# Optimization experiments

Measured on AMD Instinct MI355X. Metric: run time of the kernel, lower is better.

## Reference

```python
import jax, jax.numpy as jnp
import numpy as np

TEMPERATURE = 8.0  # sqrt(d_k) with d_k = 64


def setup_inputs() -> dict:
    key = jax.random.key(0)
    kq, kk, kv = jax.random.split(key, 3)
    B, L, D = 64, 1024, 64
    q = jax.random.normal(kq, (B, L, D), dtype=jnp.float32)
    k = jax.random.normal(kk, (B, L, D), dtype=jnp.float32)
    v = jax.random.normal(kv, (B, L, D), dtype=jnp.float32)
    return {"q": q, "k": k, "v": v}


def reference(q, k, v):
    # attn = q @ k^T / temperature  -> [B, Lq, Lk]
    attn = jnp.einsum("bqd,bkd->bqk", q, k) / TEMPERATURE
    attn = jax.nn.softmax(attn, axis=2)
    # output = attn @ v -> [B, Lq, Dv]  (dropout is identity in eval mode)
    out = jnp.einsum("bqk,bkd->bqd", attn, v)
    return out
```

## Files before the change

### kernel.cpp

```cpp
#include <hip/hip_runtime.h>
#include <hip/hip_bf16.h>

#define L_SEQ 1024
#define NT 32

typedef __attribute__((ext_vector_type(8))) __bf16 bf16x8;
typedef __attribute__((ext_vector_type(4))) __bf16 bf16x4;
typedef __attribute__((ext_vector_type(4))) float f32x4;

__device__ __forceinline__ float fast_exp2(float x) {
#if __has_builtin(__builtin_amdgcn_exp2f)
    return __builtin_amdgcn_exp2f(x);
#else
    return exp2f(x);
#endif
}

#define MFMA16(a, b, c) __builtin_amdgcn_mfma_f32_16x16x32_bf16((a), (b), (c), 0, 0, 0)

__global__ __launch_bounds__(512) void sdpa_fused(
    const float* __restrict__ Q, const float* __restrict__ K,
    const float* __restrict__ V, float* __restrict__ O)
{
    __shared__ __align__(16) char lds[2 * 8192];

    const int tid  = threadIdx.x;
    const int lane = tid & 63;
    const int wave = tid >> 6;
    const int li   = lane & 15;
    const int h    = lane >> 4;

    const int wg = blockIdx.x;
    const int lb = (wg & 7) * 64 + (wg >> 3);
    const int b  = lb >> 3;
    const int qt = lb & 7;
    const int q0 = qt * 128 + wave * 16 + li;

    const float* Qb = Q + (size_t)b * L_SEQ * 64;
    const char*  Kb = (const char*)(K + (size_t)b * L_SEQ * 64);
    const float* Vf = V + (size_t)b * L_SEQ * 64;

    int kd0;
    {
        const int qi = tid;
        const int r  = qi >> 4;
        const int d4 = (qi & 15) << 2;
        const int c32 = d4 >> 5, rem = d4 & 31, hf = rem >> 4, hh = (rem & 15) >> 2;
        kd0 = r * 128 + 2 * (((c32 * 32 + hh * 8) ^ ((r & 7) * 8)) + hf * 4);
    }
    const int vd  = tid & 63;
    const int vwd = 4096 + vd * 64 + 8 * (wave ^ ((vd >> 1) & 7));

    const float QSC = 0.18033688011112042f;
    bf16x8 qf0, qf1;
    {
        const float* ra = &Qb[(size_t)q0 * 64];
        f32x4 a00 = *(const f32x4*)&ra[0  + h * 4];
        f32x4 a01 = *(const f32x4*)&ra[16 + h * 4];
        f32x4 a10 = *(const f32x4*)&ra[32 + h * 4];
        f32x4 a11 = *(const f32x4*)&ra[48 + h * 4];
        #pragma unroll
        for (int j = 0; j < 4; ++j) {
            qf0[j]     = (__bf16)(a00[j] * QSC);
            qf0[4 + j] = (__bf16)(a01[j] * QSC);
            qf1[j]     = (__bf16)(a10[j] * QSC);
            qf1[4 + j] = (__bf16)(a11[j] * QSC);
        }
    }

    bf16x8 ones;
    #pragma unroll
    for (int j = 0; j < 8; ++j) ones[j] = (__bf16)1.0f;

    const float NBIAS = -46.0f;
    f32x4 o0 = {0.f,0.f,0.f,0.f}, o1 = {0.f,0.f,0.f,0.f};
    f32x4 o2 = {0.f,0.f,0.f,0.f}, o3 = {0.f,0.f,0.f,0.f};
    f32x4 ol = {0.f,0.f,0.f,0.f};

    f32x4 sk0, sv0;
    auto load = [&](int t) {
        const size_t tb = (size_t)t * 8192;
        sk0 = *(const f32x4*)(Kb + tb + (tid << 4));
        const float* vcol = Vf + (size_t)t * 2048 + (size_t)(wave * 4) * 64 + vd;
        #pragma unroll
        for (int u = 0; u < 4; ++u) sv0[u] = vcol[u * 64];
    };
    auto writebuf = [&](int bi) {
        char* B = lds + bi * 8192;
        bf16x4 a, v0;
        #pragma unroll
        for (int j = 0; j < 4; ++j) { a[j] = (__bf16)sk0[j]; v0[j] = (__bf16)sv0[j]; }
        *(bf16x4*)(B + kd0) = a;
        *(bf16x4*)(B + vwd) = v0;
    };

    const int kswz = (li & 7) << 4;
    const int swr  = (li >> 1) & 7;
    const int vo   = (h ^ swr) << 3;

    auto body = [&](int bi) {
        const char* bb = lds + bi * 8192;
        bf16x8 kf00 = *(const bf16x8*)(bb + li * 128 + ((h * 16) ^ kswz));
        bf16x8 kf01 = *(const bf16x8*)(bb + li * 128 + ((64 + h * 16) ^ kswz));
        bf16x8 kf10 = *(const bf16x8*)(bb + 2048 + li * 128 + ((h * 16) ^ kswz));
        bf16x8 kf11 = *(const bf16x8*)(bb + 2048 + li * 128 + ((64 + h * 16) ^ kswz));
        bf16x8 vf[4];
        #pragma unroll
        for (int dc = 0; dc < 4; ++dc) {
            const char* vbase = bb + 4096 + (dc * 16 + li) * 64;
            bf16x4 lo = *(const bf16x4*)(vbase + vo);
            bf16x4 hi = *(const bf16x4*)(vbase + (vo ^ 32));
            vf[dc] = __builtin_shufflevector(lo, hi, 0, 1, 2, 3, 4, 5, 6, 7);
        }

        const f32x4 nb = {NBIAS, NBIAS, NBIAS, NBIAS};
        f32x4 s0 = MFMA16(kf01, qf1, MFMA16(kf00, qf0, nb));
        f32x4 s1 = MFMA16(kf11, qf1, MFMA16(kf10, qf0, nb));

        bf16x8 pf;
        #pragma unroll
        for (int r = 0; r < 4; ++r) {
            pf[r]     = (__bf16)fast_exp2(s0[r]);
            pf[4 + r] = (__bf16)fast_exp2(s1[r]);
        }

        o0 = MFMA16(vf[0], pf, o0);
        o1 = MFMA16(vf[1], pf, o1);
        o2 = MFMA16(vf[2], pf, o2);
        o3 = MFMA16(vf[3], pf, o3);
        ol = MFMA16(ones, pf, ol);
    };

    auto fence_barrier = [&]() {
        asm volatile("s_waitcnt lgkmcnt(0)" ::: "memory");
        __builtin_amdgcn_s_barrier();
    };

    load(0);
    writebuf(0);
    load(1);
    fence_barrier();

    #pragma unroll 2
    for (int t = 0; t < NT - 2; ++t) {
        writebuf((t + 1) & 1);
        load(t + 2);
        body(t & 1);
        fence_barrier();
    }
    writebuf(31 & 1);
    body(30 & 1);
    fence_barrier();
    body(31 & 1);

    const float inv_l = 1.f / ol[0];

    float* Ob = O + ((size_t)b * L_SEQ + q0) * 64;
    f32x4 ov;
    #pragma unroll
    for (int r = 0; r < 4; ++r) ov[r] = o0[r] * inv_l;
    *(f32x4*)&Ob[0 * 16 + h * 4] = ov;
    #pragma unroll
    for (int r = 0; r < 4; ++r) ov[r] = o1[r] * inv_l;
    *(f32x4*)&Ob[1 * 16 + h * 4] = ov;
    #pragma unroll
    for (int r = 0; r < 4; ++r) ov[r] = o2[r] * inv_l;
    *(f32x4*)&Ob[2 * 16 + h * 4] = ov;
    #pragma unroll
    for (int r = 0; r < 4; ++r) ov[r] = o3[r] * inv_l;
    *(f32x4*)&Ob[3 * 16 + h * 4] = ov;
}

extern "C" void kernel_launch(void* const* d_in, const int* in_sizes, int n_in,
                              void* d_out, int out_size, void* d_ws, size_t ws_size,
                              hipStream_t stream) {
    const float* q = (const float*)d_in[0];
    const float* k = (const float*)d_in[1];
    const float* v = (const float*)d_in[2];
    float* o = (float*)d_out;

    sdpa_fused<<<dim3(512), dim3(512), 0, stream>>>(q, k, v, o);
}
```

Measured before the change: 33.00 us.

## Use 1024-thread blocks covering 256 queries with split K/V staging threads

Each workgroup now processes 256 queries with 16 waves instead of 128 queries with 8 waves, halving the grid to 256 blocks. Each K/V tile loaded into LDS is therefore reused by twice as many query rows, which halves the global K/V traffic and the conversion work per query. Staging is split so the first 512 threads load and convert K and the other 512 load and convert V. The cost is 256 blocks on a GPU with 256 CUs, larger barrier groups, and tighter register limits under the 1024-thread launch bound.

```diff
diff --git a/kernel.cpp b/kernel.cpp
--- a/kernel.cpp
+++ b/kernel.cpp
@@ -18,7 +18,7 @@
 
 #define MFMA16(a, b, c) __builtin_amdgcn_mfma_f32_16x16x32_bf16((a), (b), (c), 0, 0, 0)
 
-__global__ __launch_bounds__(512) void sdpa_fused(
+__global__ __launch_bounds__(1024) void sdpa_fused(
     const float* __restrict__ Q, const float* __restrict__ K,
     const float* __restrict__ V, float* __restrict__ O)
 {
@@ -31,25 +31,30 @@
     const int h    = lane >> 4;
 
     const int wg = blockIdx.x;
-    const int lb = (wg & 7) * 64 + (wg >> 3);
-    const int b  = lb >> 3;
-    const int qt = lb & 7;
-    const int q0 = qt * 128 + wave * 16 + li;
+    const int lb = (wg & 7) * 32 + (wg >> 3);
+    const int b  = lb >> 2;
+    const int qt = lb & 3;
+    const int q0 = qt * 256 + wave * 16 + li;
 
     const float* Qb = Q + (size_t)b * L_SEQ * 64;
     const char*  Kb = (const char*)(K + (size_t)b * L_SEQ * 64);
     const float* Vf = V + (size_t)b * L_SEQ * 64;
 
-    int kd0;
-    {
+    const bool kstager = (tid < 512);
+    int wd;
+    int vd = 0, vrow = 0;
+    if (kstager) {
         const int qi = tid;
         const int r  = qi >> 4;
         const int d4 = (qi & 15) << 2;
         const int c32 = d4 >> 5, rem = d4 & 31, hf = rem >> 4, hh = (rem & 15) >> 2;
-        kd0 = r * 128 + 2 * (((c32 * 32 + hh * 8) ^ ((r & 7) * 8)) + hf * 4);
+        wd = r * 128 + 2 * (((c32 * 32 + hh * 8) ^ ((r & 7) * 8)) + hf * 4);
+    } else {
+        const int vt = tid - 512;
+        vd   = vt & 63;
+        vrow = (vt >> 6) * 4;
+        wd = 4096 + vd * 64 + 8 * ((vt >> 6) ^ ((vd >> 1) & 7));
     }
-    const int vd  = tid & 63;
-    const int vwd = 4096 + vd * 64 + 8 * (wave ^ ((vd >> 1) & 7));
 
     const float QSC = 0.18033688011112042f;
     bf16x8 qf0, qf1;
@@ -77,21 +82,21 @@
     f32x4 o2 = {0.f,0.f,0.f,0.f}, o3 = {0.f,0.f,0.f,0.f};
     f32x4 ol = {0.f,0.f,0.f,0.f};
 
-    f32x4 sk0, sv0;
+    f32x4 sk0;
     auto load = [&](int t) {
-        const size_t tb = (size_t)t * 8192;
-        sk0 = *(const f32x4*)(Kb + tb + (tid << 4));
-        const float* vcol = Vf + (size_t)t * 2048 + (size_t)(wave * 4) * 64 + vd;
-        #pragma unroll
-        for (int u = 0; u < 4; ++u) sv0[u] = vcol[u * 64];
+        if (kstager) {
+            sk0 = *(const f32x4*)(Kb + (size_t)t * 8192 + (tid << 4));
+        } else {
+            const float* vcol = Vf + (size_t)t * 2048 + (size_t)vrow * 64 + vd;
+            #pragma unroll
+            for (int u = 0; u < 4; ++u) sk0[u] = vcol[u * 64];
+        }
     };
     auto writebuf = [&](int bi) {
-        char* B = lds + bi * 8192;
-        bf16x4 a, v0;
+        bf16x4 a;
         #pragma unroll
-        for (int j = 0; j < 4; ++j) { a[j] = (__bf16)sk0[j]; v0[j] = (__bf16)sv0[j]; }
-        *(bf16x4*)(B + kd0) = a;
-        *(bf16x4*)(B + vwd) = v0;
+        for (int j = 0; j < 4; ++j) a[j] = (__bf16)sk0[j];
+        *(bf16x4*)(lds + bi * 8192 + wd) = a;
     };
 
     const int kswz = (li & 7) << 4;
@@ -179,5 +184,5 @@
     const float* v = (const float*)d_in[2];
     float* o = (float*)d_out;
 
-    sdpa_fused<<<dim3(512), dim3(512), 0, stream>>>(q, k, v, o);
+    sdpa_fused<<<dim3(256), dim3(1024), 0, stream>>>(q, k, v, o);
 }
```

New measurement: 33.27 us. Within noise of the previous version (+0.8%).
